# Optimization experiments

Hardware: AMD Instinct MI355X
Metric: run time of the kernel (lower is better)

The kernel has to match this reference:

```python
import jax, jax.numpy as jnp
import numpy as np


def setup_inputs() -> dict:
    key = jax.random.key(0)
    k1, k2 = jax.random.split(key)
    B, T, C, N = 8, 4096, 512, 512
    x = jax.random.normal(k1, (B, T, C), dtype=jnp.float32)
    # regions in 1..N (docstring: region indices start from 1)
    regions = jax.random.randint(k2, (B, T), 0, N) + 1
    regions = regions.astype(jnp.int64)
    return {"x": x, "regions": regions, "max_n": N}


def reference(x, regions, max_n):
    # x: [..., T, C]; regions: int [..., T] in 1..max_n
    N = max_n
    idx = jnp.arange(N + 1)  # [N+1]
    # region_map: [..., N+1, T] one-hot comparison matrix
    region_map = idx[:, None] == regions[..., None, :]
    region_weight = region_map.astype(x.dtype)
    # segment size, clamped to 1 for empty segments
    region_size = jnp.where(
        jnp.any(region_map, axis=-1, keepdims=True),
        jnp.sum(region_weight, axis=-1, keepdims=True),
        jnp.asarray(1.0, x.dtype),
    )
    weight = region_weight / region_size  # mean-pooling weights
    weight = weight[..., 1:, :]  # drop region 0 -> [..., N, T]
    # segment mean via matmul: [..., N, T] @ [..., T, C] -> [..., N, C]
    return weight @ x
```

## Files before the change

### kernel.cpp

```cpp
#include <hip/hip_runtime.h>


#define B_   8
#define T_   4096
#define C_   512
#define N_   512

__global__ __launch_bounds__(1024) void prep_kernel(
    const int* __restrict__ regions,
    int* __restrict__ counts_g,
    int* __restrict__ offs_g,
    int* __restrict__ list_g)
{
    __shared__ int cnts[N_];
    __shared__ int scan[N_];
    __shared__ int cursor[N_];

    const int b   = blockIdx.x;
    const int tid = threadIdx.x;

    if (tid < N_) cnts[tid] = 0;
    __syncthreads();

    int rloc[T_ / 1024];
#pragma unroll
    for (int k = 0; k < T_ / 1024; ++k) {
        const int t  = tid + k * 1024;
        const int rv = regions[b * T_ + t] - 1;
        rloc[k] = rv;
        if ((unsigned)rv < (unsigned)N_) atomicAdd(&cnts[rv], 1);
    }
    __syncthreads();

    if (tid < N_) scan[tid] = cnts[tid];
    __syncthreads();
    for (int d = 1; d < N_; d <<= 1) {
        int v = 0;
        if (tid < N_ && tid >= d) v = scan[tid - d];
        __syncthreads();
        if (tid < N_) scan[tid] += v;
        __syncthreads();
    }

    if (tid < N_) {
        const int e = scan[tid] - cnts[tid];
        cursor[tid] = e;
        offs_g  [b * N_ + tid] = e;
        counts_g[b * N_ + tid] = cnts[tid];
    }
    __syncthreads();

#pragma unroll
    for (int k = 0; k < T_ / 1024; ++k) {
        const int t  = tid + k * 1024;
        const int rv = rloc[k];
        if ((unsigned)rv < (unsigned)N_) {
            const int pos = atomicAdd(&cursor[rv], 1);
            list_g[b * T_ + pos] = t;
        }
    }
}

__global__ __launch_bounds__(128) void mean_kernel(
    const float* __restrict__ x,
    const int*   __restrict__ counts_g,
    const int*   __restrict__ offs_g,
    const int*   __restrict__ list_g,
    float*       __restrict__ out)
{
    const int bn  = blockIdx.x;
    const int b   = bn >> 9;
    const int tid = threadIdx.x;

    const int cnt = counts_g[bn];
    const int off = offs_g[bn];
    const int* __restrict__ lst = list_g + b * T_ + off;

    const float4* __restrict__ x4 =
        reinterpret_cast<const float4*>(x) + (size_t)b * T_ * (C_ / 4);

    float4 a0 = {0.f, 0.f, 0.f, 0.f};
    float4 a1 = {0.f, 0.f, 0.f, 0.f};
    float4 a2 = {0.f, 0.f, 0.f, 0.f};
    float4 a3 = {0.f, 0.f, 0.f, 0.f};

    int i = 0;
    for (; i + 4 <= cnt; i += 4) {
        const int t0 = lst[i + 0];
        const int t1 = lst[i + 1];
        const int t2 = lst[i + 2];
        const int t3 = lst[i + 3];
        const float4 v0 = x4[(size_t)t0 * (C_ / 4) + tid];
        const float4 v1 = x4[(size_t)t1 * (C_ / 4) + tid];
        const float4 v2 = x4[(size_t)t2 * (C_ / 4) + tid];
        const float4 v3 = x4[(size_t)t3 * (C_ / 4) + tid];
        a0.x += v0.x; a0.y += v0.y; a0.z += v0.z; a0.w += v0.w;
        a1.x += v1.x; a1.y += v1.y; a1.z += v1.z; a1.w += v1.w;
        a2.x += v2.x; a2.y += v2.y; a2.z += v2.z; a2.w += v2.w;
        a3.x += v3.x; a3.y += v3.y; a3.z += v3.z; a3.w += v3.w;
    }
    for (; i < cnt; ++i) {
        const int t = lst[i];
        const float4 v = x4[(size_t)t * (C_ / 4) + tid];
        a0.x += v.x; a0.y += v.y; a0.z += v.z; a0.w += v.w;
    }

    float4 s;
    s.x = (a0.x + a1.x) + (a2.x + a3.x);
    s.y = (a0.y + a1.y) + (a2.y + a3.y);
    s.z = (a0.z + a1.z) + (a2.z + a3.z);
    s.w = (a0.w + a1.w) + (a2.w + a3.w);

    const float scale = (cnt > 0) ? (1.0f / (float)cnt) : 0.0f;
    s.x *= scale; s.y *= scale; s.z *= scale; s.w *= scale;

    reinterpret_cast<float4*>(out)[(size_t)bn * (C_ / 4) + tid] = s;
}

extern "C" void kernel_launch(void* const* d_in, const int* in_sizes, int n_in,
                              void* d_out, int out_size, void* d_ws, size_t ws_size,
                              hipStream_t stream)
{
    const float* x       = (const float*)d_in[0];
    const int*   regions = (const int*)d_in[1];

    int* counts = (int*)d_ws;
    int* offs   = counts + B_ * N_;
    int* list   = offs   + B_ * N_;

    prep_kernel<<<B_, 1024, 0, stream>>>(regions, counts, offs, list);
    mean_kernel<<<B_ * N_, 128, 0, stream>>>(x, counts, offs, list, (float*)d_out);
}
```

Baseline: 101.3 us.

## Fuse region bucketing into mean kernel via per-block region scan

Drops the separate prep kernel that built a global sorted index list with counts and offsets. Each (batch, region) block now scans the whole region row of its batch, collects matching token indices into a shared-memory list with a shared atomic counter, then gathers and averages the x rows. This removes one launch and the serialized 8-block prep phase. In exchange every block rereads the 16KB region row, so region reads grow by a factor of N, and the list order becomes nondeterministic, which can change float summation order.

New measurement: 98.45 us. -2.8%, faster.

```diff
diff --git a/kernel.cpp b/kernel.cpp
--- a/kernel.cpp
+++ b/kernel.cpp
@@ -6,75 +6,36 @@
 #define C_   512
 #define N_   512
 
-__global__ __launch_bounds__(1024) void prep_kernel(
-    const int* __restrict__ regions,
-    int* __restrict__ counts_g,
-    int* __restrict__ offs_g,
-    int* __restrict__ list_g)
+__global__ __launch_bounds__(128) void fused_mean_kernel(
+    const float* __restrict__ x,
+    const int*   __restrict__ regions,
+    float*       __restrict__ out)
 {
-    __shared__ int cnts[N_];
-    __shared__ int scan[N_];
-    __shared__ int cursor[N_];
+    __shared__ int list[T_];
+    __shared__ int cnt_s;
 
-    const int b   = blockIdx.x;
+    const int bn  = blockIdx.x;
+    const int b   = bn >> 9;
+    const int n   = bn & (N_ - 1);
     const int tid = threadIdx.x;
+    const int target = n + 1;
 
-    if (tid < N_) cnts[tid] = 0;
+    if (tid == 0) cnt_s = 0;
     __syncthreads();
 
-    int rloc[T_ / 1024];
+    const int4* __restrict__ r4 = reinterpret_cast<const int4*>(regions + b * T_);
 #pragma unroll
-    for (int k = 0; k < T_ / 1024; ++k) {
-        const int t  = tid + k * 1024;
-        const int rv = regions[b * T_ + t] - 1;
-        rloc[k] = rv;
-        if ((unsigned)rv < (unsigned)N_) atomicAdd(&cnts[rv], 1);
+    for (int k = 0; k < T_ / (4 * 128); ++k) {
+        const int  idx = tid + k * 128;
+        const int4 rv  = r4[idx];
+        const int  t0  = idx * 4;
+        if (rv.x == target) list[atomicAdd(&cnt_s, 1)] = t0;
+        if (rv.y == target) list[atomicAdd(&cnt_s, 1)] = t0 + 1;
+        if (rv.z == target) list[atomicAdd(&cnt_s, 1)] = t0 + 2;
+        if (rv.w == target) list[atomicAdd(&cnt_s, 1)] = t0 + 3;
     }
     __syncthreads();
-
-    if (tid < N_) scan[tid] = cnts[tid];
-    __syncthreads();
-    for (int d = 1; d < N_; d <<= 1) {
-        int v = 0;
-        if (tid < N_ && tid >= d) v = scan[tid - d];
-        __syncthreads();
-        if (tid < N_) scan[tid] += v;
-        __syncthreads();
-    }
-
-    if (tid < N_) {
-        const int e = scan[tid] - cnts[tid];
-        cursor[tid] = e;
-        offs_g  [b * N_ + tid] = e;
-        counts_g[b * N_ + tid] = cnts[tid];
-    }
-    __syncthreads();
-
-#pragma unroll
-    for (int k = 0; k < T_ / 1024; ++k) {
-        const int t  = tid + k * 1024;
-        const int rv = rloc[k];
-        if ((unsigned)rv < (unsigned)N_) {
-            const int pos = atomicAdd(&cursor[rv], 1);
-            list_g[b * T_ + pos] = t;
-        }
-    }
-}
-
-__global__ __launch_bounds__(128) void mean_kernel(
-    const float* __restrict__ x,
-    const int*   __restrict__ counts_g,
-    const int*   __restrict__ offs_g,
-    const int*   __restrict__ list_g,
-    float*       __restrict__ out)
-{
-    const int bn  = blockIdx.x;
-    const int b   = bn >> 9;
-    const int tid = threadIdx.x;
-
-    const int cnt = counts_g[bn];
-    const int off = offs_g[bn];
-    const int* __restrict__ lst = list_g + b * T_ + off;
+    const int cnt = cnt_s;
 
     const float4* __restrict__ x4 =
         reinterpret_cast<const float4*>(x) + (size_t)b * T_ * (C_ / 4);
@@ -86,10 +47,10 @@
 
     int i = 0;
     for (; i + 4 <= cnt; i += 4) {
-        const int t0 = lst[i + 0];
-        const int t1 = lst[i + 1];
-        const int t2 = lst[i + 2];
-        const int t3 = lst[i + 3];
+        const int t0 = list[i + 0];
+        const int t1 = list[i + 1];
+        const int t2 = list[i + 2];
+        const int t3 = list[i + 3];
         const float4 v0 = x4[(size_t)t0 * (C_ / 4) + tid];
         const float4 v1 = x4[(size_t)t1 * (C_ / 4) + tid];
         const float4 v2 = x4[(size_t)t2 * (C_ / 4) + tid];
@@ -100,7 +61,7 @@
         a3.x += v3.x; a3.y += v3.y; a3.z += v3.z; a3.w += v3.w;
     }
     for (; i < cnt; ++i) {
-        const int t = lst[i];
+        const int t = list[i];
         const float4 v = x4[(size_t)t * (C_ / 4) + tid];
         a0.x += v.x; a0.y += v.y; a0.z += v.z; a0.w += v.w;
     }
@@ -124,10 +85,5 @@
     const float* x       = (const float*)d_in[0];
     const int*   regions = (const int*)d_in[1];
 
-    int* counts = (int*)d_ws;
-    int* offs   = counts + B_ * N_;
-    int* list   = offs   + B_ * N_;
-
-    prep_kernel<<<B_, 1024, 0, stream>>>(regions, counts, offs, list);
-    mean_kernel<<<B_ * N_, 128, 0, stream>>>(x, counts, offs, list, (float*)d_out);
+    fused_mean_kernel<<<B_ * N_, 128, 0, stream>>>(x, regions, (float*)d_out);
 }
```
